# Performance work log

Hardware: AMD Instinct MI355X
Metric: run time of the kernel (lower is better)

Reference implementation:

```python
import jax, jax.numpy as jnp
import numpy as np

N_NODES = 20000
N_EDGES = 640000
H = 64            # node_hidden_size
E_FEAT = 16       # edge_features_size
T = 2             # num_prop_rounds


def setup_inputs() -> dict:
    key = jax.random.key(0)
    ks = jax.random.split(key, 10)
    hv = jax.random.normal(ks[0], (N_NODES, H), dtype=jnp.float32)
    e = jax.random.normal(ks[1], (N_EDGES, E_FEAT), dtype=jnp.float32)
    src = jax.random.randint(ks[2], (N_EDGES,), 0, N_NODES, dtype=jnp.int32)
    dst = jax.random.randint(ks[3], (N_EDGES,), 0, N_NODES, dtype=jnp.int32)
    s = 0.1  # param init scale to keep activations in a sane range
    W_msg = jax.random.normal(ks[4], (T, 2 * H + E_FEAT, 2 * H), dtype=jnp.float32) * s
    b_msg = jax.random.normal(ks[5], (T, 2 * H), dtype=jnp.float32) * s
    W_ih = jax.random.normal(ks[6], (T, 3 * H, 2 * H), dtype=jnp.float32) * s
    W_hh = jax.random.normal(ks[7], (T, 3 * H, H), dtype=jnp.float32) * s
    b_ih = jax.random.normal(ks[8], (T, 3 * H), dtype=jnp.float32) * s
    b_hh = jax.random.normal(ks[9], (T, 3 * H), dtype=jnp.float32) * s
    return {"hv": hv, "e": e, "src": src, "dst": dst,
            "W_msg": W_msg, "b_msg": b_msg,
            "W_ih": W_ih, "W_hh": W_hh, "b_ih": b_ih, "b_hh": b_hh}


def _gru_cell(a, h, W_ih, W_hh, b_ih, b_hh):
    # torch.nn.GRUCell math
    gi = a @ W_ih.T + b_ih   # [N, 3H]
    gh = h @ W_hh.T + b_hh   # [N, 3H]
    i_r, i_z, i_n = jnp.split(gi, 3, axis=1)
    h_r, h_z, h_n = jnp.split(gh, 3, axis=1)
    r = jax.nn.sigmoid(i_r + h_r)
    z = jax.nn.sigmoid(i_z + h_z)
    n = jnp.tanh(i_n + r * h_n)
    return (1.0 - z) * n + z * h


def reference(hv, e, src, dst, W_msg, b_msg, W_ih, W_hh, b_ih, b_hh):
    num_nodes = hv.shape[0]
    num_rounds = W_msg.shape[0]
    for t in range(num_rounds):  # small fixed loop over prop rounds
        # per-edge: concat([h_dst, h_src, e_uv]) -> Linear -> sum-reduce to dst
        msg_in = jnp.concatenate([hv[dst], hv[src], e], axis=1)  # [E, 2H+Ef]
        msgs = msg_in @ W_msg[t] + b_msg[t]                      # [E, 2H]
        a = jax.ops.segment_sum(msgs, dst, num_segments=num_nodes)  # [N, 2H]
        hv = _gru_cell(a, hv, W_ih[t], W_hh[t], b_ih[t], b_hh[t])
    return hv
```

## Files before the change

### kernel.cpp

```cpp
#include <hip/hip_runtime.h>
#include <cstddef>
#include <cstdint>

#define NN 20000
#define NE 640000
#define MP 20096
#define KA 224
#define NC 8
#define CHUNK 80000
#define NB_SCAN 79

typedef _Float16 f16x8 __attribute__((ext_vector_type(8)));
typedef float f32x4 __attribute__((ext_vector_type(4)));

__device__ __forceinline__ float h2f(unsigned short u) {
    _Float16 h;
    *reinterpret_cast<unsigned short*>(&h) = u;
    return (float)h;
}
__device__ __forceinline__ unsigned short f2h(float f) {
    _Float16 h = (_Float16)f;
    return *reinterpret_cast<unsigned short*>(&h);
}
__device__ __forceinline__ void splitf(float x, unsigned short& hi, unsigned short& lo) {
    _Float16 h = (_Float16)x;
    _Float16 l = (_Float16)(x - (float)h);
    hi = *reinterpret_cast<unsigned short*>(&h);
    lo = *reinterpret_cast<unsigned short*>(&l);
}

__global__ void zero_kernel(int* __restrict__ p, int n) {
    int i = blockIdx.x * blockDim.x + threadIdx.x;
    if (i < n) p[i] = 0;
}

__global__ void tohf_kernel(const float* __restrict__ in, unsigned short* __restrict__ out, int n) {
    int i = blockIdx.x * blockDim.x + threadIdx.x;
    if (i < n) out[i] = f2h(in[i]);
}

__global__ void hist_kernel(const int* __restrict__ dst, int* __restrict__ cnt) {
    int i = blockIdx.x * blockDim.x + threadIdx.x;
    if (i < NE) atomicAdd(&cnt[(i / CHUNK) * NN + dst[i]], 1);
}

__global__ __launch_bounds__(256) void scan1_kernel(const int* __restrict__ cnt,
                                                    int* __restrict__ lp,
                                                    int* __restrict__ bsum) {
    __shared__ int s[256];
    int t = threadIdx.x;
    int i = blockIdx.x * 256 + t;
    int d = 0;
    if (i < NN)
#pragma unroll
        for (int c = 0; c < NC; ++c) d += cnt[c * NN + i];
    s[t] = d;
    __syncthreads();
    for (int off = 1; off < 256; off <<= 1) {
        int v = (t >= off) ? s[t - off] : 0;
        __syncthreads();
        s[t] += v;
        __syncthreads();
    }
    if (i < NN) lp[i] = s[t] - d;
    if (t == 255) bsum[blockIdx.x] = s[255];
}

__global__ __launch_bounds__(128) void scan2_kernel(const int* __restrict__ bsum,
                                                    int* __restrict__ boff) {
    __shared__ int s[128];
    int t = threadIdx.x;
    int v = (t < NB_SCAN) ? bsum[t] : 0;
    s[t] = v;
    __syncthreads();
    for (int off = 1; off < 128; off <<= 1) {
        int u = (t >= off) ? s[t - off] : 0;
        __syncthreads();
        s[t] += u;
        __syncthreads();
    }
    if (t < NB_SCAN) boff[t] = s[t] - v;
}

__global__ __launch_bounds__(256) void scan3_kernel(const int* __restrict__ cnt,
                                                    const int* __restrict__ lp,
                                                    const int* __restrict__ boff,
                                                    int* __restrict__ row_ptr,
                                                    int* __restrict__ cursor) {
    int i = blockIdx.x * 256 + threadIdx.x;
    if (i < NN) {
        int run = boff[blockIdx.x] + lp[i];
        row_ptr[i] = run;
#pragma unroll
        for (int c = 0; c < NC; ++c) {
            cursor[c * NN + i] = run;
            run += cnt[c * NN + i];
        }
    }
    if (i == 0) row_ptr[NN] = NE;
}

__global__ void place_kernel(const int* __restrict__ src, const int* __restrict__ dst,
                             int* __restrict__ cursor, int2* __restrict__ adj) {
    int i = blockIdx.x * blockDim.x + threadIdx.x;
    if (i < NE) {
        int d = dst[i];
        int pos = atomicAdd(&cursor[(i / CHUNK) * NN + d], 1);
        adj[pos] = make_int2(src[i], i);
    }
}

__global__ __launch_bounds__(256) void esum_csr_kernel(
        const float* __restrict__ ef, const int* __restrict__ row_ptr,
        const int2* __restrict__ adj, float* __restrict__ esum,
        float* __restrict__ degf) {
    int wid = threadIdx.x >> 6, lane = threadIdx.x & 63;
    int v = blockIdx.x * 4 + wid;
    if (v >= NN) return;
    int rp0 = row_ptr[v], rp1 = row_ptr[v + 1];
    int q = lane >> 2;
    int fo = (lane & 3) << 2;
    float4 a0 = make_float4(0.f, 0.f, 0.f, 0.f), a1 = a0;
    int i = rp0 + q;
    for (; i + 16 < rp1; i += 32) {
        int e0 = adj[i].y, e1 = adj[i + 16].y;
        float4 x0 = *(const float4*)(ef + (size_t)e0 * 16 + fo);
        float4 x1 = *(const float4*)(ef + (size_t)e1 * 16 + fo);
        a0.x += x0.x; a0.y += x0.y; a0.z += x0.z; a0.w += x0.w;
        a1.x += x1.x; a1.y += x1.y; a1.z += x1.z; a1.w += x1.w;
    }
    for (; i < rp1; i += 16) {
        int e = adj[i].y;
        float4 x = *(const float4*)(ef + (size_t)e * 16 + fo);
        a0.x += x.x; a0.y += x.y; a0.z += x.z; a0.w += x.w;
    }
    a0.x += a1.x; a0.y += a1.y; a0.z += a1.z; a0.w += a1.w;
#pragma unroll
    for (int m = 4; m < 64; m <<= 1) {
        a0.x += __shfl_xor(a0.x, m);
        a0.y += __shfl_xor(a0.y, m);
        a0.z += __shfl_xor(a0.z, m);
        a0.w += __shfl_xor(a0.w, m);
    }
    if (lane < 4) *(float4*)(esum + (size_t)v * 16 + fo) = a0;
    if (lane == 0) degf[v] = (float)(rp1 - rp0);
}

__global__ __launch_bounds__(192) void fold_kernel(
        const float* __restrict__ W_msg, const float* __restrict__ b_msg,
        const float* __restrict__ W_ih, float* __restrict__ WcT,
        float* __restrict__ bvec) {
    __shared__ float ldsW[64][193];
    int t = blockIdx.x / 9;
    int k0 = (blockIdx.x % 9) * 16;
    int j = threadIdx.x;
    float acc[16];
#pragma unroll
    for (int kk = 0; kk < 16; ++kk) acc[kk] = 0.f;
    float bacc = 0.f;
    for (int mc = 0; mc < 2; ++mc) {
        for (int i = threadIdx.x; i < 192 * 64; i += 192) {
            int jj = i >> 6, mm = i & 63;
            ldsW[mm][jj] = W_ih[((size_t)t * 192 + jj) * 128 + mc * 64 + mm];
        }
        __syncthreads();
        for (int mm = 0; mm < 64; ++mm) {
            float wl = ldsW[mm][j];
            float bm = b_msg[t * 128 + mc * 64 + mm];
            bacc = fmaf(bm, wl, bacc);
#pragma unroll
            for (int kk = 0; kk < 16; ++kk) {
                float wm = W_msg[((size_t)t * 144 + k0 + kk) * 128 + mc * 64 + mm];
                acc[kk] = fmaf(wm, wl, acc[kk]);
            }
        }
        __syncthreads();
    }
#pragma unroll
    for (int kk = 0; kk < 16; ++kk)
        WcT[((size_t)t * 192 + j) * 144 + k0 + kk] = acc[kk];
    if (k0 == 0) bvec[t * 192 + j] = bacc;
}

__global__ void wbig_kernel(const float* __restrict__ WcT, const float* __restrict__ bvec,
                            const float* __restrict__ b_ih, const float* __restrict__ b_hh,
                            const float* __restrict__ W_hh,
                            unsigned short* __restrict__ Bhi, unsigned short* __restrict__ Blo) {
    int idx = blockIdx.x * 256 + threadIdx.x;
    if (idx >= 2 * 256 * KA) return;
    int t = idx / (256 * KA);
    int rem = idx % (256 * KA);
    int n = rem / KA, k = rem % KA;
    float v = 0.f;
    if (n < 192) {
        if (k < 64) {
            if (n < 128) v = W_hh[(size_t)t * 192 * 64 + n * 64 + k];
        } else if (k < 128) {
            v = WcT[((size_t)t * 192 + n) * 144 + k];
        } else if (k < 192) {
            v = WcT[((size_t)t * 192 + n) * 144 + (k - 128)];
        } else if (k < 208) {
            v = WcT[((size_t)t * 192 + n) * 144 + 128 + (k - 192)];
        } else if (k == 208) {
            v = bvec[t * 192 + n];
        } else if (k == 209) {
            v = (n < 128) ? (b_ih[t * 192 + n] + b_hh[t * 192 + n]) : b_ih[t * 192 + n];
        }
    } else {
        int j = n - 64;
        if (k < 64) v = W_hh[(size_t)t * 192 * 64 + j * 64 + k];
        else if (k == 209) v = b_hh[t * 192 + j];
    }
    unsigned short hi, lo;
    splitf(v, hi, lo);
    Bhi[idx] = hi;
    Blo[idx] = lo;
}

__global__ void atail_kernel(const float* __restrict__ esum, const float* __restrict__ degf,
                             unsigned short* __restrict__ Ahi, unsigned short* __restrict__ Alo) {
    int i = blockIdx.x * blockDim.x + threadIdx.x;
    if (i >= NN * 32) return;
    int v = i >> 5, k = 192 + (i & 31);
    float val;
    if (k < 208) val = esum[(size_t)v * 16 + (k - 192)];
    else if (k == 208) val = degf[v];
    else if (k == 209) val = 1.f;
    else val = 0.f;
    unsigned short hi, lo;
    splitf(val, hi, lo);
    Ahi[(size_t)v * KA + k] = hi;
    Alo[(size_t)v * KA + k] = lo;
}

__global__ __launch_bounds__(256) void gather_kernel(
        const float* __restrict__ hv, const unsigned short* __restrict__ hf,
        const int* __restrict__ row_ptr, const int2* __restrict__ adj,
        unsigned short* __restrict__ Ahi, unsigned short* __restrict__ Alo) {
    int wid = threadIdx.x >> 6, lane = threadIdx.x & 63;
    int v = blockIdx.x * 4 + wid;
    if (v >= NN) return;
    int rp0 = row_ptr[v], rp1 = row_ptr[v + 1];
    int q = lane >> 4;
    int fo = (lane & 15) << 2;
    float4 acc[8];
#pragma unroll
    for (int u = 0; u < 8; ++u) acc[u] = make_float4(0.f, 0.f, 0.f, 0.f);
    int i = rp0 + q;
    for (; i + 28 < rp1; i += 32) {
        int s[8];
#pragma unroll
        for (int u = 0; u < 8; ++u) s[u] = adj[i + 4 * u].x;
#pragma unroll
        for (int u = 0; u < 8; ++u) {
            ushort4 x = *(const ushort4*)(hf + (size_t)s[u] * 64 + fo);
            acc[u].x += h2f(x.x); acc[u].y += h2f(x.y);
            acc[u].z += h2f(x.z); acc[u].w += h2f(x.w);
        }
    }
    for (; i + 4 < rp1; i += 8) {
        int s0 = adj[i].x, s1 = adj[i + 4].x;
        ushort4 x0 = *(const ushort4*)(hf + (size_t)s0 * 64 + fo);
        ushort4 x1 = *(const ushort4*)(hf + (size_t)s1 * 64 + fo);
        acc[0].x += h2f(x0.x); acc[0].y += h2f(x0.y);
        acc[0].z += h2f(x0.z); acc[0].w += h2f(x0.w);
        acc[1].x += h2f(x1.x); acc[1].y += h2f(x1.y);
        acc[1].z += h2f(x1.z); acc[1].w += h2f(x1.w);
    }
    for (; i < rp1; i += 4) {
        int s = adj[i].x;
        ushort4 x = *(const ushort4*)(hf + (size_t)s * 64 + fo);
        acc[0].x += h2f(x.x); acc[0].y += h2f(x.y);
        acc[0].z += h2f(x.z); acc[0].w += h2f(x.w);
    }
#pragma unroll
    for (int u = 1; u < 8; ++u) {
        acc[0].x += acc[u].x; acc[0].y += acc[u].y;
        acc[0].z += acc[u].z; acc[0].w += acc[u].w;
    }
#pragma unroll
    for (int m = 16; m < 64; m <<= 1) {
        acc[0].x += __shfl_xor(acc[0].x, m);
        acc[0].y += __shfl_xor(acc[0].y, m);
        acc[0].z += __shfl_xor(acc[0].z, m);
        acc[0].w += __shfl_xor(acc[0].w, m);
    }
    if (lane < 16) {
        float dg = (float)(rp1 - rp0);
        float4 hvv = *(const float4*)(hv + (size_t)v * 64 + fo);
        float4 dv = make_float4(dg * hvv.x, dg * hvv.y, dg * hvv.z, dg * hvv.w);
        ushort4 hh, hl, sh, sl, dh, dl;
        splitf(hvv.x, hh.x, hl.x); splitf(hvv.y, hh.y, hl.y);
        splitf(hvv.z, hh.z, hl.z); splitf(hvv.w, hh.w, hl.w);
        splitf(acc[0].x, sh.x, sl.x); splitf(acc[0].y, sh.y, sl.y);
        splitf(acc[0].z, sh.z, sl.z); splitf(acc[0].w, sh.w, sl.w);
        splitf(dv.x, dh.x, dl.x); splitf(dv.y, dh.y, dl.y);
        splitf(dv.z, dh.z, dl.z); splitf(dv.w, dh.w, dl.w);
        *(ushort4*)(Ahi + (size_t)v * KA + fo) = hh;
        *(ushort4*)(Alo + (size_t)v * KA + fo) = hl;
        *(ushort4*)(Ahi + (size_t)v * KA + 64 + fo) = sh;
        *(ushort4*)(Alo + (size_t)v * KA + 64 + fo) = sl;
        *(ushort4*)(Ahi + (size_t)v * KA + 128 + fo) = dh;
        *(ushort4*)(Alo + (size_t)v * KA + 128 + fo) = dl;
    }
}

__global__ __launch_bounds__(512) void gemm_gru(
        const _Float16* __restrict__ Ahi, const _Float16* __restrict__ Alo,
        const _Float16* __restrict__ Bhi, const _Float16* __restrict__ Blo,
        const float* __restrict__ hin,
        float* __restrict__ fout, unsigned short* __restrict__ hfout) {
    __shared__ _Float16 Ash[128][40];
    __shared__ _Float16 Asl[128][40];
    __shared__ _Float16 Bsh[256][40];
    __shared__ _Float16 Bsl[256][40];
    int tid = threadIdx.x;
    int w = tid >> 6, l = tid & 63;
    int row0 = blockIdx.x * 128;
    f32x4 acc[16];
#pragma unroll
    for (int i = 0; i < 16; ++i) acc[i] = (f32x4){0.f, 0.f, 0.f, 0.f};

#pragma unroll 1
    for (int ks = 0; ks < 7; ++ks) {
        int k0 = ks * 32;
        {
            int r = tid >> 2, c = (tid & 3) * 8;
            *(float4*)&Ash[r][c] = *(const float4*)(Ahi + (size_t)(row0 + r) * KA + k0 + c);
            *(float4*)&Asl[r][c] = *(const float4*)(Alo + (size_t)(row0 + r) * KA + k0 + c);
        }
        {
            int n = tid >> 1, c = (tid & 1) * 16;
            const float4* ph = (const float4*)(Bhi + (size_t)n * KA + k0 + c);
            float4 h0 = ph[0], h1 = ph[1];
            *(float4*)&Bsh[n][c] = h0;
            *(float4*)&Bsh[n][c + 8] = h1;
            const float4* pl = (const float4*)(Blo + (size_t)n * KA + k0 + c);
            float4 l0 = pl[0], l1 = pl[1];
            *(float4*)&Bsl[n][c] = l0;
            *(float4*)&Bsl[n][c + 8] = l1;
        }
        __syncthreads();
        int kg = (l >> 4) * 8;
        int ar = w * 16 + (l & 15);
        f16x8 ah = *(const f16x8*)&Ash[ar][kg];
        f16x8 al = *(const f16x8*)&Asl[ar][kg];
#pragma unroll
        for (int fn = 0; fn < 16; ++fn) {
            f16x8 bh = *(const f16x8*)&Bsh[fn * 16 + (l & 15)][kg];
            f16x8 bl = *(const f16x8*)&Bsl[fn * 16 + (l & 15)][kg];
            acc[fn] = __builtin_amdgcn_mfma_f32_16x16x32_f16(ah, bh, acc[fn], 0, 0, 0);
            acc[fn] = __builtin_amdgcn_mfma_f32_16x16x32_f16(ah, bl, acc[fn], 0, 0, 0);
            acc[fn] = __builtin_amdgcn_mfma_f32_16x16x32_f16(al, bh, acc[fn], 0, 0, 0);
        }
        __syncthreads();
    }

    int jb = l & 15;
#pragma unroll
    for (int q = 0; q < 4; ++q) {
        int row = row0 + w * 16 + (l >> 4) * 4 + q;
        if (row >= NN) continue;
#pragma unroll
        for (int fj = 0; fj < 4; ++fj) {
            int j = jb + fj * 16;
            float rr = acc[fj][q];
            float zz = acc[4 + fj][q];
            float in_ = acc[8 + fj][q];
            float hn = acc[12 + fj][q];
            float r = 1.f / (1.f + __expf(-rr));
            float z = 1.f / (1.f + __expf(-zz));
            float n = tanhf(in_ + r * hn);
            float h = hin[(size_t)row * 64 + j];
            float val = (1.f - z) * n + z * h;
            fout[(size_t)row * 64 + j] = val;
            hfout[(size_t)row * 64 + j] = f2h(val);
        }
    }
}

extern "C" void kernel_launch(void* const* d_in, const int* in_sizes, int n_in,
                              void* d_out, int out_size, void* d_ws, size_t ws_size,
                              hipStream_t stream) {
    const float* hv0   = (const float*)d_in[0];
    const float* ef    = (const float*)d_in[1];
    const int*   src   = (const int*)d_in[2];
    const int*   dst   = (const int*)d_in[3];
    const float* W_msg = (const float*)d_in[4];
    const float* b_msg = (const float*)d_in[5];
    const float* W_ih  = (const float*)d_in[6];
    const float* W_hh  = (const float*)d_in[7];
    const float* b_ih  = (const float*)d_in[8];
    const float* b_hh  = (const float*)d_in[9];
    float* out = (float*)d_out;

    char* ws = (char*)d_ws;
    size_t off = 0;
    auto alloc = [&](size_t bytes) -> char* {
        char* p = ws + off;
        off = (off + bytes + 255) & ~(size_t)255;
        return p;
    };
    int*   cnt      = (int*)alloc((size_t)NC * NN * 4);
    int*   row_ptr  = (int*)alloc((NN + 1) * 4);
    int*   cursor   = (int*)alloc((size_t)NC * NN * 4);
    int2*  adj      = (int2*)alloc((size_t)NE * 8);
    float* esum     = (float*)alloc((size_t)NN * 16 * 4);
    float* degf     = (float*)alloc(NN * 4);
    float* WcT      = (float*)alloc((size_t)2 * 192 * 144 * 4);
    float* bvec     = (float*)alloc(2 * 192 * 4);
    int*   lp       = (int*)alloc(NN * 4);
    int*   bsum     = (int*)alloc(NB_SCAN * 4);
    int*   boff     = (int*)alloc(NB_SCAN * 4);
    unsigned short* Ahi = (unsigned short*)alloc((size_t)MP * KA * 2);
    unsigned short* Alo = (unsigned short*)alloc((size_t)MP * KA * 2);
    unsigned short* Bhi = (unsigned short*)alloc((size_t)2 * 256 * KA * 2);
    unsigned short* Blo = (unsigned short*)alloc((size_t)2 * 256 * KA * 2);
    float* hv1      = (float*)alloc((size_t)NN * 64 * 4);
    unsigned short* hf0 = (unsigned short*)alloc((size_t)NN * 64 * 2);
    unsigned short* hf1 = (unsigned short*)alloc((size_t)NN * 64 * 2);

    zero_kernel<<<(NC * NN + 1023) / 1024, 1024, 0, stream>>>(cnt, NC * NN);
    tohf_kernel<<<(NN * 64 + 255) / 256, 256, 0, stream>>>(hv0, hf0, NN * 64);
    hist_kernel<<<(NE + 255) / 256, 256, 0, stream>>>(dst, cnt);
    scan1_kernel<<<NB_SCAN, 256, 0, stream>>>(cnt, lp, bsum);
    scan2_kernel<<<1, 128, 0, stream>>>(bsum, boff);
    scan3_kernel<<<NB_SCAN, 256, 0, stream>>>(cnt, lp, boff, row_ptr, cursor);
    place_kernel<<<(NE + 255) / 256, 256, 0, stream>>>(src, dst, cursor, adj);
    esum_csr_kernel<<<(NN + 3) / 4, 256, 0, stream>>>(ef, row_ptr, adj, esum, degf);
    fold_kernel<<<18, 192, 0, stream>>>(W_msg, b_msg, W_ih, WcT, bvec);
    wbig_kernel<<<(2 * 256 * KA + 255) / 256, 256, 0, stream>>>(WcT, bvec, b_ih, b_hh,
                                                                W_hh, Bhi, Blo);
    atail_kernel<<<(NN * 32 + 255) / 256, 256, 0, stream>>>(esum, degf, Ahi, Alo);

    for (int t = 0; t < 2; ++t) {
        const float* hin = (t == 0) ? hv0 : hv1;
        const unsigned short* hfin = (t == 0) ? hf0 : hf1;
        float* hout = (t == 1) ? out : hv1;
        gather_kernel<<<(NN + 3) / 4, 256, 0, stream>>>(hin, hfin, row_ptr, adj, Ahi, Alo);
        gemm_gru<<<MP / 128, 512, 0, stream>>>(
            (const _Float16*)Ahi, (const _Float16*)Alo,
            (const _Float16*)(Bhi + (size_t)t * 256 * KA),
            (const _Float16*)(Blo + (size_t)t * 256 * KA),
            hin, hout, hf1);
    }
}
```

Before: 213.3 us.

## Merge setup kernels, fold scan2 into scan3, shrink GEMM tile, double histogram chunks

Combines zeroing and fp16 conversion into one init kernel and folds the block-offset scan into scan3, so each scan3 block rescans the block sums itself. Together these remove two launches. Doubles the histogram chunk count to spread atomic contention. Halves the gemm_gru row tile to 64 rows with 256 threads, doubling block count to improve occupancy and CU coverage. In exchange, B tiles are reloaded by twice as many blocks and the counter arrays grow.

```diff
diff --git a/kernel.cpp b/kernel.cpp
--- a/kernel.cpp
+++ b/kernel.cpp
@@ -6,8 +6,8 @@
 #define NE 640000
 #define MP 20096
 #define KA 224
-#define NC 8
-#define CHUNK 80000
+#define NC 16
+#define CHUNK 40000
 #define NB_SCAN 79
 
 typedef _Float16 f16x8 __attribute__((ext_vector_type(8)));
@@ -29,14 +29,11 @@
     lo = *reinterpret_cast<unsigned short*>(&l);
 }
 
-__global__ void zero_kernel(int* __restrict__ p, int n) {
+__global__ void init_kernel(const float* __restrict__ hv0, unsigned short* __restrict__ hf0,
+                            int* __restrict__ cnt) {
     int i = blockIdx.x * blockDim.x + threadIdx.x;
-    if (i < n) p[i] = 0;
-}
-
-__global__ void tohf_kernel(const float* __restrict__ in, unsigned short* __restrict__ out, int n) {
-    int i = blockIdx.x * blockDim.x + threadIdx.x;
-    if (i < n) out[i] = f2h(in[i]);
+    if (i < NC * NN) cnt[i] = 0;
+    if (i < NN * 64) hf0[i] = f2h(hv0[i]);
 }
 
 __global__ void hist_kernel(const int* __restrict__ dst, int* __restrict__ cnt) {
@@ -66,30 +63,25 @@
     if (t == 255) bsum[blockIdx.x] = s[255];
 }
 
-__global__ __launch_bounds__(128) void scan2_kernel(const int* __restrict__ bsum,
-                                                    int* __restrict__ boff) {
-    __shared__ int s[128];
+__global__ __launch_bounds__(256) void scan3_kernel(const int* __restrict__ cnt,
+                                                    const int* __restrict__ lp,
+                                                    const int* __restrict__ bsum,
+                                                    int* __restrict__ row_ptr,
+                                                    int* __restrict__ cursor) {
+    __shared__ int sb[128];
     int t = threadIdx.x;
-    int v = (t < NB_SCAN) ? bsum[t] : 0;
-    s[t] = v;
+    if (t < 128) sb[t] = (t < NB_SCAN) ? bsum[t] : 0;
     __syncthreads();
     for (int off = 1; off < 128; off <<= 1) {
-        int u = (t >= off) ? s[t - off] : 0;
-        __syncthreads();
-        s[t] += u;
-        __syncthreads();
-    }
-    if (t < NB_SCAN) boff[t] = s[t] - v;
-}
-
-__global__ __launch_bounds__(256) void scan3_kernel(const int* __restrict__ cnt,
-                                                    const int* __restrict__ lp,
-                                                    const int* __restrict__ boff,
-                                                    int* __restrict__ row_ptr,
-                                                    int* __restrict__ cursor) {
-    int i = blockIdx.x * 256 + threadIdx.x;
+        int u = (t < 128 && t >= off) ? sb[t - off] : 0;
+        __syncthreads();
+        if (t < 128) sb[t] += u;
+        __syncthreads();
+    }
+    int boff = (blockIdx.x == 0) ? 0 : sb[blockIdx.x - 1];
+    int i = blockIdx.x * 256 + t;
     if (i < NN) {
-        int run = boff[blockIdx.x] + lp[i];
+        int run = boff + lp[i];
         row_ptr[i] = run;
 #pragma unroll
         for (int c = 0; c < NC; ++c) {
@@ -305,18 +297,18 @@
     }
 }
 
-__global__ __launch_bounds__(512) void gemm_gru(
+__global__ __launch_bounds__(256) void gemm_gru(
         const _Float16* __restrict__ Ahi, const _Float16* __restrict__ Alo,
         const _Float16* __restrict__ Bhi, const _Float16* __restrict__ Blo,
         const float* __restrict__ hin,
         float* __restrict__ fout, unsigned short* __restrict__ hfout) {
-    __shared__ _Float16 Ash[128][40];
-    __shared__ _Float16 Asl[128][40];
+    __shared__ _Float16 Ash[64][40];
+    __shared__ _Float16 Asl[64][40];
     __shared__ _Float16 Bsh[256][40];
     __shared__ _Float16 Bsl[256][40];
     int tid = threadIdx.x;
     int w = tid >> 6, l = tid & 63;
-    int row0 = blockIdx.x * 128;
+    int row0 = blockIdx.x * 64;
     f32x4 acc[16];
 #pragma unroll
     for (int i = 0; i < 16; ++i) acc[i] = (f32x4){0.f, 0.f, 0.f, 0.f};
@@ -330,15 +322,15 @@
             *(float4*)&Asl[r][c] = *(const float4*)(Alo + (size_t)(row0 + r) * KA + k0 + c);
         }
         {
-            int n = tid >> 1, c = (tid & 1) * 16;
-            const float4* ph = (const float4*)(Bhi + (size_t)n * KA + k0 + c);
-            float4 h0 = ph[0], h1 = ph[1];
-            *(float4*)&Bsh[n][c] = h0;
-            *(float4*)&Bsh[n][c + 8] = h1;
-            const float4* pl = (const float4*)(Blo + (size_t)n * KA + k0 + c);
-            float4 l0 = pl[0], l1 = pl[1];
-            *(float4*)&Bsl[n][c] = l0;
-            *(float4*)&Bsl[n][c + 8] = l1;
+            int n = tid;
+            const float4* ph = (const float4*)(Bhi + (size_t)n * KA + k0);
+            float4 h0 = ph[0], h1 = ph[1], h2 = ph[2], h3 = ph[3];
+            *(float4*)&Bsh[n][0] = h0;  *(float4*)&Bsh[n][8] = h1;
+            *(float4*)&Bsh[n][16] = h2; *(float4*)&Bsh[n][24] = h3;
+            const float4* pl = (const float4*)(Blo + (size_t)n * KA + k0);
+            float4 l0 = pl[0], l1 = pl[1], l2 = pl[2], l3 = pl[3];
+            *(float4*)&Bsl[n][0] = l0;  *(float4*)&Bsl[n][8] = l1;
+            *(float4*)&Bsl[n][16] = l2; *(float4*)&Bsl[n][24] = l3;
         }
         __syncthreads();
         int kg = (l >> 4) * 8;
@@ -411,7 +403,6 @@
     float* bvec     = (float*)alloc(2 * 192 * 4);
     int*   lp       = (int*)alloc(NN * 4);
     int*   bsum     = (int*)alloc(NB_SCAN * 4);
-    int*   boff     = (int*)alloc(NB_SCAN * 4);
     unsigned short* Ahi = (unsigned short*)alloc((size_t)MP * KA * 2);
     unsigned short* Alo = (unsigned short*)alloc((size_t)MP * KA * 2);
     unsigned short* Bhi = (unsigned short*)alloc((size_t)2 * 256 * KA * 2);
@@ -420,12 +411,10 @@
     unsigned short* hf0 = (unsigned short*)alloc((size_t)NN * 64 * 2);
     unsigned short* hf1 = (unsigned short*)alloc((size_t)NN * 64 * 2);
 
-    zero_kernel<<<(NC * NN + 1023) / 1024, 1024, 0, stream>>>(cnt, NC * NN);
-    tohf_kernel<<<(NN * 64 + 255) / 256, 256, 0, stream>>>(hv0, hf0, NN * 64);
+    init_kernel<<<(NN * 64 + 255) / 256, 256, 0, stream>>>(hv0, hf0, cnt);
     hist_kernel<<<(NE + 255) / 256, 256, 0, stream>>>(dst, cnt);
     scan1_kernel<<<NB_SCAN, 256, 0, stream>>>(cnt, lp, bsum);
-    scan2_kernel<<<1, 128, 0, stream>>>(bsum, boff);
-    scan3_kernel<<<NB_SCAN, 256, 0, stream>>>(cnt, lp, boff, row_ptr, cursor);
+    scan3_kernel<<<NB_SCAN, 256, 0, stream>>>(cnt, lp, bsum, row_ptr, cursor);
     place_kernel<<<(NE + 255) / 256, 256, 0, stream>>>(src, dst, cursor, adj);
     esum_csr_kernel<<<(NN + 3) / 4, 256, 0, stream>>>(ef, row_ptr, adj, esum, degf);
     fold_kernel<<<18, 192, 0, stream>>>(W_msg, b_msg, W_ih, WcT, bvec);
@@ -438,7 +427,7 @@
         const unsigned short* hfin = (t == 0) ? hf0 : hf1;
         float* hout = (t == 1) ? out : hv1;
         gather_kernel<<<(NN + 3) / 4, 256, 0, stream>>>(hin, hfin, row_ptr, adj, Ahi, Alo);
-        gemm_gru<<<MP / 128, 512, 0, stream>>>(
+        gemm_gru<<<MP / 64, 256, 0, stream>>>(
             (const _Float16*)Ahi, (const _Float16*)Alo,
             (const _Float16*)(Bhi + (size_t)t * 256 * KA),
             (const _Float16*)(Blo + (size_t)t * 256 * KA),
```

After: 207.1 us. 1.03x faster.
